# Kernel optimization log

Measured on AMD Instinct MI355X. Metric: run time of the kernel, lower is better.

Reference implementation:

```python
import jax, jax.numpy as jnp
import numpy as np

CR = 0.8
THRESH_FACTOR = 0.05
BN_EPS = 1e-5
NEG_SLOPE = 0.2

@jax.custom_vjp
def ternary(weight, pos, neg):
    # TWN-style ternarization: thresh = f * max|W|
    t = THRESH_FACTOR * jnp.max(jnp.abs(weight))
    pos_i = (weight > t).astype(weight.dtype)
    neg_i = (weight < -t).astype(weight.dtype)
    return pos * pos_i + neg * neg_i

def _tern_fwd(weight, pos, neg):
    t = THRESH_FACTOR * jnp.max(jnp.abs(weight))
    pos_i = (weight > t).astype(weight.dtype)
    neg_i = (weight < -t).astype(weight.dtype)
    return pos * pos_i + neg * neg_i, (pos_i, neg_i, pos, neg)

def _tern_bwd(res, g):
    # matches torch Function_ternary.backward (STE-style)
    pos_i, neg_i, pos, neg = res
    pruned = 1.0 - pos_i - neg_i
    grad_w = pos * g * pos_i + g * pruned + neg * g * neg_i
    return grad_w, jnp.mean(g * pos_i), jnp.mean(g * neg_i)

ternary.defvjp(_tern_fwd, _tern_bwd)

def setup_inputs() -> dict:
    key = jax.random.key(0)
    ks = jax.random.split(key, 6)
    B, Cin, H, W = 32, 256, 64, 64
    Cout, K = 512, 4
    return {
        "x": jax.random.normal(ks[0], (B, Cin, H, W), jnp.float32),
        "weight": jax.random.normal(ks[1], (Cout, Cin, K, K), jnp.float32) * 0.05,
        "pos": jax.random.uniform(ks[2], (), jnp.float32),
        "neg": -jax.random.uniform(ks[3], (), jnp.float32),
        "sal_w": jax.random.normal(ks[4], (Cout, Cin), jnp.float32) * 0.05,
        "sal_b": jax.random.normal(ks[5], (Cout,), jnp.float32) * 0.01,
        "gamma": jnp.ones((Cout,), jnp.float32),
        "beta": jnp.zeros((Cout,), jnp.float32),
    }

def reference(x, weight, pos, neg, sal_w, sal_b, gamma, beta):
    Cout = weight.shape[0]
    # FBS: per-sample channel saliency from spatially pooled |x|
    sub = jnp.mean(jnp.abs(x), axis=(2, 3))                 # [B, Cin]
    sal = jnp.abs(sub @ sal_w.T + sal_b)                    # [B, Cout]
    k = int(np.round(Cout * CR))
    thr = jax.lax.top_k(sal, k)[0][:, -1]                   # k-th largest per sample
    mask = sal * (sal > thr[:, None]).astype(x.dtype)       # [B, Cout]
    # ternary-quantized conv, stride 2, pad 1 (hardcoded in source)
    tw = ternary(weight, pos, neg)
    y = jax.lax.conv_general_dilated(
        x, tw, window_strides=(2, 2), padding=[(1, 1), (1, 1)],
        dimension_numbers=("NCHW", "OIHW", "NCHW"))          # [B, Cout, 32, 32]
    y = mask[:, :, None, None] * y
    # BatchNorm2d (training-mode batch statistics, eps=1e-5)
    mu = jnp.mean(y, axis=(0, 2, 3), keepdims=True)
    var = jnp.var(y, axis=(0, 2, 3), keepdims=True)
    y = (y - mu) * jax.lax.rsqrt(var + BN_EPS)
    y = y * gamma[None, :, None, None] + beta[None, :, None, None]
    # LeakyReLU(0.2)
    return jnp.where(y > 0, y, NEG_SLOPE * y)
```

## Files before the change

### kernel.cpp

```cpp
#include <hip/hip_runtime.h>
#include <stdint.h>

typedef __attribute__((ext_vector_type(8))) short short8;
typedef __attribute__((ext_vector_type(4))) float f32x4;
typedef __attribute__((ext_vector_type(4))) uint32_t u32x4;
typedef __attribute__((ext_vector_type(4))) unsigned short u16x4;

#define K_TOP 410

#define WS_ABSMAX 0
#define WS_GSUM   1024
#define WS_GSQ    3072
#define WS_SCALE  5120
#define WS_SHIFT  7168
#define WS_SUB    16384
#define WS_MASK   65536
#define WS_BMAT   131072

__device__ __forceinline__ unsigned short f2bf(float f) {
  uint32_t u = __float_as_uint(f);
  u += 0x7fffu + ((u >> 16) & 1u);
  return (unsigned short)(u >> 16);
}

__device__ __forceinline__ uint32_t pkbf(float a, float b) {
  uint32_t r;
  asm("v_cvt_pk_bf16_f32 %0, %1, %2" : "=v"(r) : "v"(a), "v"(b));
  return r;
}

__global__ void k_sub(const float* __restrict__ x, float* __restrict__ sub) {
  int bid = blockIdx.x;
  const f32x4* xp = (const f32x4*)(x + (size_t)bid * 4096);
  int t = threadIdx.x;
  float s = 0.f;
#pragma unroll
  for (int i = 0; i < 4; ++i) {
    f32x4 v = xp[t + i * 256];
    s += fabsf(v.x) + fabsf(v.y) + fabsf(v.z) + fabsf(v.w);
  }
#pragma unroll
  for (int off = 32; off > 0; off >>= 1) s += __shfl_xor(s, off);
  __shared__ float red[4];
  if ((t & 63) == 0) red[t >> 6] = s;
  __syncthreads();
  if (t == 0) sub[bid] = (red[0] + red[1] + red[2] + red[3]) * (1.f / 4096.f);
}

__global__ void k_wmax(const float* __restrict__ w, unsigned int* __restrict__ wsmax) {
  int t = blockIdx.x * 256 + threadIdx.x;
  const f32x4* wp = (const f32x4*)w;
  float m = 0.f;
#pragma unroll
  for (int i = 0; i < 8; ++i) {
    f32x4 v = wp[t + i * 65536];
    m = fmaxf(m, fmaxf(fmaxf(fabsf(v.x), fabsf(v.y)), fmaxf(fabsf(v.z), fabsf(v.w))));
  }
#pragma unroll
  for (int off = 32; off > 0; off >>= 1) m = fmaxf(m, __shfl_xor(m, off));
  __shared__ float red[4];
  if ((threadIdx.x & 63) == 0) red[threadIdx.x >> 6] = m;
  __syncthreads();
  if (threadIdx.x == 0) {
    m = fmaxf(fmaxf(red[0], red[1]), fmaxf(red[2], red[3]));
    atomicMax(wsmax, __float_as_uint(m));
  }
}

__global__ void k_mask(const float* __restrict__ sub, const float* __restrict__ salw,
                       const float* __restrict__ salb, float* __restrict__ mask) {
  int b = blockIdx.x, n = threadIdx.x;
  __shared__ float subs[256];
  __shared__ float sals[512];
  __shared__ float thr_s;
  if (n < 256) subs[n] = sub[b * 256 + n];
  __syncthreads();
  float acc = salb[n];
#pragma unroll 4
  for (int c = 0; c < 256; ++c) acc += subs[c] * salw[n * 256 + c];
  float sal = fabsf(acc);
  sals[n] = sal;
  __syncthreads();
  int gt = 0, eq = 0;
  for (int j = 0; j < 512; ++j) {
    float v = sals[j];
    gt += (v > sal);
    eq += (v == sal);
  }
  if (gt < K_TOP && gt + eq >= K_TOP) thr_s = sal;
  __syncthreads();
  mask[b * 512 + n] = (sal > thr_s) ? sal : 0.f;
}

__global__ void k_quant(const float* __restrict__ w, const unsigned int* __restrict__ wsmax,
                        const float* __restrict__ posp, const float* __restrict__ negp,
                        unsigned short* __restrict__ bmat2) {
  int id = blockIdx.x * 256 + threadIdx.x;
  int c = id & 2047;
  int ktq = (id >> 11) & 63;
  int ntq = id >> 17;
  int n = c >> 3, sp = c & 7;
  int s = sp ^ (n & 7);
  int cout = ntq * 256 + n;
  const float* src = w + (size_t)cout * 4096 + ktq * 64 + s * 8;
  float thr = 0.05f * __uint_as_float(*wsmax);
  unsigned short bp = f2bf(*posp), bn = f2bf(*negp);
  f32x4 a = *(const f32x4*)src;
  f32x4 bq = *(const f32x4*)(src + 4);
  u16x4 q0, q1;
  q0.x = a.x > thr ? bp : (a.x < -thr ? bn : (unsigned short)0);
  q0.y = a.y > thr ? bp : (a.y < -thr ? bn : (unsigned short)0);
  q0.z = a.z > thr ? bp : (a.z < -thr ? bn : (unsigned short)0);
  q0.w = a.w > thr ? bp : (a.w < -thr ? bn : (unsigned short)0);
  q1.x = bq.x > thr ? bp : (bq.x < -thr ? bn : (unsigned short)0);
  q1.y = bq.y > thr ? bp : (bq.y < -thr ? bn : (unsigned short)0);
  q1.z = bq.z > thr ? bp : (bq.z < -thr ? bn : (unsigned short)0);
  q1.w = bq.w > thr ? bp : (bq.w < -thr ? bn : (unsigned short)0);
  ((u16x4*)bmat2)[id * 2]     = q0;
  ((u16x4*)bmat2)[id * 2 + 1] = q1;
}

__launch_bounds__(512, 2)
__global__ void k_gemm(const float* __restrict__ x, const unsigned short* __restrict__ bmat2,
                       const float* __restrict__ mask, float* __restrict__ out,
                       float* __restrict__ gsum, float* __restrict__ gsq) {
  __shared__ __align__(16) unsigned short xsL[2][36 * 32 * 8];
  __shared__ __align__(16) unsigned short bsL[2][2048 * 8];

  int tid = threadIdx.x;
  int lane = tid & 63, wid = tid >> 6;
  int wm = wid >> 2, wn = wid & 3;
  int g = lane >> 4, lr = lane & 15;

  int wg = blockIdx.x;
  int nt = wg & 1, mt = wg >> 1;
  int b = mt >> 2, OH0 = (mt & 3) * 8;
  const size_t xb = (size_t)b * 256 * 4096;

  int jA = tid & 15, riA = tid >> 4;
  int c2A = riA / 9, rpA = riA - c2A * 9;
  int ihA = 2 * (OH0 + rpA) - 1;
  bool vA0 = (unsigned)ihA < 64u, vA1 = (unsigned)(ihA + 1) < 64u;
  const float* pA = x + xb + (size_t)c2A * 4096 + (long)ihA * 64 + 4 * jA;
  bool hasB = (wid < 4) && (lane < 16);
  int riB = 32 + wid, jB = lane;
  int rpB = riB - 27;
  int ihB = 2 * (OH0 + rpB) - 1;
  bool vB0 = (unsigned)ihB < 64u, vB1 = (unsigned)(ihB + 1) < 64u;
  const float* pB = x + xb + (size_t)3 * 4096 + (long)ihB * 64 + 4 * jB;

  f32x4 acc[8][4];
#pragma unroll
  for (int i = 0; i < 8; ++i)
#pragma unroll
    for (int j = 0; j < 4; ++j) acc[i][j] = (f32x4){0.f, 0.f, 0.f, 0.f};

  auto ldrow = [&](const float* p, bool v, int j, f32x4& vv, float& pw, float& nx) {
    vv = (f32x4){0.f, 0.f, 0.f, 0.f}; pw = 0.f; nx = 0.f;
    if (v) {
      vv = *(const f32x4*)p;
      if (j != 0)  pw = p[-1];
      if (j != 15) nx = p[4];
    }
  };
  auto wtask = [&](int buf, int rowidx, int j, const f32x4& v0, const f32x4& v1,
                   float pw0, float nx0, float pw1, float nx1) {
    uint32_t a0 = pkbf(pw0, v0.x), b0 = pkbf(v0.y, v0.z), c0 = pkbf(v0.w, nx0);
    uint32_t a1 = pkbf(pw1, v1.x), b1 = pkbf(v1.y, v1.z), c1 = pkbf(v1.w, nx1);
    u32x4* dst = (u32x4*)&xsL[buf][0];
    dst[rowidx * 32 + j]      = (u32x4){a0, b0, a1, b1};
    dst[rowidx * 32 + 16 + j] = (u32x4){b0, c0, b1, c1};
  };
  auto stageB = [&](int buf, int kt) {
    size_t gbase = (size_t)(nt * 64 + kt) * 2048 * 8;
    int wbase = tid & ~63;
#pragma unroll
    for (int q = 0; q < 4; ++q) {
      __builtin_amdgcn_global_load_lds(
          (const uint32_t*)(bmat2 + gbase + (size_t)(q * 512 + tid) * 8),
          (uint32_t*)&bsL[buf][(size_t)(q * 512 + wbase) * 8], 16, 0, 0);
    }
  };

  {
    f32x4 t0v0, t0v1, t1v0, t1v1;
    float t0pw0, t0nx0, t0pw1, t0nx1, t1pw0, t1nx0, t1pw1, t1nx1;
    ldrow(pA, vA0, jA, t0v0, t0pw0, t0nx0);
    ldrow(pA + 64, vA1, jA, t0v1, t0pw1, t0nx1);
    if (hasB) {
      ldrow(pB, vB0, jB, t1v0, t1pw0, t1nx0);
      ldrow(pB + 64, vB1, jB, t1v1, t1pw1, t1nx1);
    }
    stageB(0, 0);
    wtask(0, riA, jA, t0v0, t0v1, t0pw0, t0nx0, t0pw1, t0nx1);
    if (hasB) wtask(0, riB, jB, t1v0, t1v1, t1pw0, t1nx0, t1pw1, t1nx1);
  }
  __syncthreads();

  union UF { u32x4 u; short8 s; };

  for (int kt = 0; kt < 64; ++kt) {
    int cur = kt & 1, nxt = cur ^ 1;

    f32x4 t0v0, t0v1, t1v0, t1v1;
    float t0pw0, t0nx0, t0pw1, t0nx1, t1pw0, t1nx0, t1pw1, t1nx1;
    if (kt < 63) {
      const float* p0 = pA + (size_t)(kt + 1) * 16384;
      ldrow(p0, vA0, jA, t0v0, t0pw0, t0nx0);
      ldrow(p0 + 64, vA1, jA, t0v1, t0pw1, t0nx1);
      if (hasB) {
        const float* p1 = pB + (size_t)(kt + 1) * 16384;
        ldrow(p1, vB0, jB, t1v0, t1pw0, t1nx0);
        ldrow(p1 + 64, vB1, jB, t1v1, t1pw1, t1nx1);
      }
      stageB(nxt, kt + 1);
    }

    const u32x4* xp4 = (const u32x4*)&xsL[cur][0];
    const u32x4* bp4 = (const u32x4*)&bsL[cur][0];
#pragma unroll
    for (int kk = 0; kk < 2; ++kk) {
      UF bf[4];
#pragma unroll
      for (int ni = 0; ni < 4; ++ni) {
        int nloc = wn * 64 + ni * 16 + lr;
        bf[ni].u = bp4[nloc * 8 + ((4 * kk + g) ^ (nloc & 7))];
      }
      __builtin_amdgcn_s_setprio(1);
#pragma unroll
      for (int mi = 0; mi < 8; ++mi) {
        int rowidx = (2 * kk + (g >> 1)) * 9 + wm * 4 + (mi >> 1) + (g & 1);
        int ow = ((mi & 1) << 4) + lr;
        UF af; af.u = xp4[rowidx * 32 + (ow >> 1) + ((ow & 1) << 4)];
#pragma unroll
        for (int ni = 0; ni < 4; ++ni)
          acc[mi][ni] = __builtin_amdgcn_mfma_f32_16x16x32_bf16(af.s, bf[ni].s, acc[mi][ni], 0, 0, 0);
      }
      __builtin_amdgcn_s_setprio(0);
    }

    if (kt < 63) {
      wtask(nxt, riA, jA, t0v0, t0v1, t0pw0, t0nx0, t0pw1, t0nx1);
      if (hasB) wtask(nxt, riB, jB, t1v0, t1v1, t1pw0, t1nx0, t1pw1, t1nx1);
    }
    __syncthreads();
  }

  float msk[4];
#pragma unroll
  for (int ni = 0; ni < 4; ++ni)
    msk[ni] = mask[b * 512 + nt * 256 + wn * 64 + ni * 16 + lr];

  float psum[4] = {0.f, 0.f, 0.f, 0.f}, psq[4] = {0.f, 0.f, 0.f, 0.f};
#pragma unroll
  for (int ni = 0; ni < 4; ++ni) {
    int n = nt * 256 + wn * 64 + ni * 16 + lr;
    float* op = out + (size_t)b * 524288 + (size_t)n * 1024 + OH0 * 32 + wm * 128 + g * 4;
#pragma unroll
    for (int mi = 0; mi < 8; ++mi) {
      f32x4 a = acc[mi][ni] * msk[ni];
      psum[ni] += a.x + a.y + a.z + a.w;
      psq[ni] += a.x * a.x + a.y * a.y + a.z * a.z + a.w * a.w;
      *(f32x4*)(op + mi * 16) = a;
    }
  }
#pragma unroll
  for (int ni = 0; ni < 4; ++ni) {
    float s = psum[ni], q = psq[ni];
    s += __shfl_xor(s, 16); s += __shfl_xor(s, 32);
    q += __shfl_xor(q, 16); q += __shfl_xor(q, 32);
    if (g == 0) {
      int n = nt * 256 + wn * 64 + ni * 16 + lr;
      atomicAdd(&gsum[n], s);
      atomicAdd(&gsq[n], q);
    }
  }
}

__global__ void k_bnprep(const float* __restrict__ gsum, const float* __restrict__ gsq,
                         const float* __restrict__ gamma, const float* __restrict__ beta,
                         float* __restrict__ scale, float* __restrict__ shift) {
  int n = threadIdx.x;
  float mu = gsum[n] * (1.f / 32768.f);
  float var = gsq[n] * (1.f / 32768.f) - mu * mu;
  float a = gamma[n] * rsqrtf(var + 1e-5f);
  scale[n] = a;
  shift[n] = beta[n] - mu * a;
}

__global__ void k_bn(float* __restrict__ y, const float* __restrict__ scale,
                     const float* __restrict__ shift) {
  int t = blockIdx.x * 256 + threadIdx.x;
  f32x4* yp = (f32x4*)y;
#pragma unroll
  for (int i = 0; i < 8; ++i) {
    int idx = t + i * 524288;
    int n = (idx >> 8) & 511;
    f32x4 v = yp[idx];
    float a = scale[n], sh = shift[n];
    v = v * a + sh;
    v.x = v.x > 0.f ? v.x : 0.2f * v.x;
    v.y = v.y > 0.f ? v.y : 0.2f * v.y;
    v.z = v.z > 0.f ? v.z : 0.2f * v.z;
    v.w = v.w > 0.f ? v.w : 0.2f * v.w;
    yp[idx] = v;
  }
}

extern "C" void kernel_launch(void* const* d_in, const int* in_sizes, int n_in,
                              void* d_out, int out_size, void* d_ws, size_t ws_size,
                              hipStream_t stream) {
  const float* x     = (const float*)d_in[0];
  const float* w     = (const float*)d_in[1];
  const float* pos   = (const float*)d_in[2];
  const float* neg   = (const float*)d_in[3];
  const float* salw  = (const float*)d_in[4];
  const float* salb  = (const float*)d_in[5];
  const float* gamma = (const float*)d_in[6];
  const float* beta  = (const float*)d_in[7];
  float* out = (float*)d_out;
  char* ws = (char*)d_ws;

  unsigned int* absmax = (unsigned int*)(ws + WS_ABSMAX);
  float* gsum  = (float*)(ws + WS_GSUM);
  float* gsq   = (float*)(ws + WS_GSQ);
  float* scale = (float*)(ws + WS_SCALE);
  float* shift = (float*)(ws + WS_SHIFT);
  float* sub   = (float*)(ws + WS_SUB);
  float* mask  = (float*)(ws + WS_MASK);
  unsigned short* bmat2 = (unsigned short*)(ws + WS_BMAT);

  hipMemsetAsync(ws, 0, 5120, stream);

  k_sub<<<8192, 256, 0, stream>>>(x, sub);
  k_wmax<<<256, 256, 0, stream>>>(w, absmax);
  k_mask<<<32, 512, 0, stream>>>(sub, salw, salb, mask);
  k_quant<<<1024, 256, 0, stream>>>(w, absmax, pos, neg, bmat2);
  k_gemm<<<256, 512, 0, stream>>>(x, bmat2, mask, out, gsum, gsq);
  k_bnprep<<<1, 512, 0, stream>>>(gsum, gsq, gamma, beta, scale, shift);
  k_bn<<<2048, 256, 0, stream>>>(out, scale, shift);
}
```

Measured before the change: 462.6 us.

## Use lane shuffles for halo values, batch LDS reads, and hand-tune barriers

The row loader now fetches only the aligned f32x4 per lane and gets the neighbouring halo elements through __shfl_up/__shfl_down, so the two scalar global loads per row go away. All A-fragments are read from LDS before the MFMA burst. __syncthreads is replaced by an explicit waitcnt, s_barrier and sched_barrier, plus an extra barrier in the middle of the k-steps. The workgroup-to-tile mapping also changes so that consecutive blocks share the same N tile instead of alternating between the two. This adds shuffle work and register pressure from holding eight A-fragments, and the extra mid-loop barrier could add stalls.

After: 419.4 us. 1.1x faster.

```diff
diff --git a/kernel.cpp b/kernel.cpp
--- a/kernel.cpp
+++ b/kernel.cpp
@@ -133,7 +133,7 @@
   int g = lane >> 4, lr = lane & 15;
 
   int wg = blockIdx.x;
-  int nt = wg & 1, mt = wg >> 1;
+  int nt = wg >> 7, mt = wg & 127;
   int b = mt >> 2, OH0 = (mt & 3) * 8;
   const size_t xb = (size_t)b * 256 * 4096;
 
@@ -143,7 +143,7 @@
   bool vA0 = (unsigned)ihA < 64u, vA1 = (unsigned)(ihA + 1) < 64u;
   const float* pA = x + xb + (size_t)c2A * 4096 + (long)ihA * 64 + 4 * jA;
   bool hasB = (wid < 4) && (lane < 16);
-  int riB = 32 + wid, jB = lane;
+  int riB = 32 + wid, jB = lane & 15;
   int rpB = riB - 27;
   int ihB = 2 * (OH0 + rpB) - 1;
   bool vB0 = (unsigned)ihB < 64u, vB1 = (unsigned)(ihB + 1) < 64u;
@@ -155,16 +155,13 @@
 #pragma unroll
     for (int j = 0; j < 4; ++j) acc[i][j] = (f32x4){0.f, 0.f, 0.f, 0.f};
 
-  auto ldrow = [&](const float* p, bool v, int j, f32x4& vv, float& pw, float& nx) {
-    vv = (f32x4){0.f, 0.f, 0.f, 0.f}; pw = 0.f; nx = 0.f;
-    if (v) {
-      vv = *(const f32x4*)p;
-      if (j != 0)  pw = p[-1];
-      if (j != 15) nx = p[4];
-    }
-  };
-  auto wtask = [&](int buf, int rowidx, int j, const f32x4& v0, const f32x4& v1,
-                   float pw0, float nx0, float pw1, float nx1) {
+  auto z4 = []() { return (f32x4){0.f, 0.f, 0.f, 0.f}; };
+
+  auto wtask = [&](int buf, int rowidx, int j, f32x4 v0, f32x4 v1) {
+    float pw0 = __shfl_up(v0.w, 1);  if (j == 0)  pw0 = 0.f;
+    float nx0 = __shfl_down(v0.x, 1); if (j == 15) nx0 = 0.f;
+    float pw1 = __shfl_up(v1.w, 1);  if (j == 0)  pw1 = 0.f;
+    float nx1 = __shfl_down(v1.x, 1); if (j == 15) nx1 = 0.f;
     uint32_t a0 = pkbf(pw0, v0.x), b0 = pkbf(v0.y, v0.z), c0 = pkbf(v0.w, nx0);
     uint32_t a1 = pkbf(pw1, v1.x), b1 = pkbf(v1.y, v1.z), c1 = pkbf(v1.w, nx1);
     u32x4* dst = (u32x4*)&xsL[buf][0];
@@ -182,36 +179,37 @@
     }
   };
 
+  union UF { u32x4 u; short8 s; };
+
   {
-    f32x4 t0v0, t0v1, t1v0, t1v1;
-    float t0pw0, t0nx0, t0pw1, t0nx1, t1pw0, t1nx0, t1pw1, t1nx1;
-    ldrow(pA, vA0, jA, t0v0, t0pw0, t0nx0);
-    ldrow(pA + 64, vA1, jA, t0v1, t0pw1, t0nx1);
+    f32x4 a0 = vA0 ? *(const f32x4*)pA : z4();
+    f32x4 a1 = vA1 ? *(const f32x4*)(pA + 64) : z4();
+    f32x4 c0 = z4(), c1 = z4();
     if (hasB) {
-      ldrow(pB, vB0, jB, t1v0, t1pw0, t1nx0);
-      ldrow(pB + 64, vB1, jB, t1v1, t1pw1, t1nx1);
+      c0 = vB0 ? *(const f32x4*)pB : z4();
+      c1 = vB1 ? *(const f32x4*)(pB + 64) : z4();
     }
     stageB(0, 0);
-    wtask(0, riA, jA, t0v0, t0v1, t0pw0, t0nx0, t0pw1, t0nx1);
-    if (hasB) wtask(0, riB, jB, t1v0, t1v1, t1pw0, t1nx0, t1pw1, t1nx1);
-  }
-  __syncthreads();
-
-  union UF { u32x4 u; short8 s; };
+    wtask(0, riA, jA, a0, a1);
+    if (hasB) wtask(0, riB, jB, c0, c1);
+    asm volatile("s_waitcnt vmcnt(0) lgkmcnt(0)" ::: "memory");
+    __builtin_amdgcn_s_barrier();
+    __builtin_amdgcn_sched_barrier(0);
+  }
 
   for (int kt = 0; kt < 64; ++kt) {
     int cur = kt & 1, nxt = cur ^ 1;
-
-    f32x4 t0v0, t0v1, t1v0, t1v1;
-    float t0pw0, t0nx0, t0pw1, t0nx1, t1pw0, t1nx0, t1pw1, t1nx1;
-    if (kt < 63) {
+    bool pre = (kt < 63);
+
+    f32x4 a0, a1, c0, c1;
+    if (pre) {
       const float* p0 = pA + (size_t)(kt + 1) * 16384;
-      ldrow(p0, vA0, jA, t0v0, t0pw0, t0nx0);
-      ldrow(p0 + 64, vA1, jA, t0v1, t0pw1, t0nx1);
+      a0 = vA0 ? *(const f32x4*)p0 : z4();
+      a1 = vA1 ? *(const f32x4*)(p0 + 64) : z4();
       if (hasB) {
         const float* p1 = pB + (size_t)(kt + 1) * 16384;
-        ldrow(p1, vB0, jB, t1v0, t1pw0, t1nx0);
-        ldrow(p1 + 64, vB1, jB, t1v1, t1pw1, t1nx1);
+        c0 = vB0 ? *(const f32x4*)p1 : z4();
+        c1 = vB1 ? *(const f32x4*)(p1 + 64) : z4();
       }
       stageB(nxt, kt + 1);
     }
@@ -226,24 +224,30 @@
         int nloc = wn * 64 + ni * 16 + lr;
         bf[ni].u = bp4[nloc * 8 + ((4 * kk + g) ^ (nloc & 7))];
       }
-      __builtin_amdgcn_s_setprio(1);
+      UF af[8];
 #pragma unroll
       for (int mi = 0; mi < 8; ++mi) {
         int rowidx = (2 * kk + (g >> 1)) * 9 + wm * 4 + (mi >> 1) + (g & 1);
         int ow = ((mi & 1) << 4) + lr;
-        UF af; af.u = xp4[rowidx * 32 + (ow >> 1) + ((ow & 1) << 4)];
+        af[mi].u = xp4[rowidx * 32 + (ow >> 1) + ((ow & 1) << 4)];
+      }
+      __builtin_amdgcn_s_setprio(1);
+#pragma unroll
+      for (int mi = 0; mi < 8; ++mi)
 #pragma unroll
         for (int ni = 0; ni < 4; ++ni)
-          acc[mi][ni] = __builtin_amdgcn_mfma_f32_16x16x32_bf16(af.s, bf[ni].s, acc[mi][ni], 0, 0, 0);
-      }
+          acc[mi][ni] = __builtin_amdgcn_mfma_f32_16x16x32_bf16(af[mi].s, bf[ni].s, acc[mi][ni], 0, 0, 0);
       __builtin_amdgcn_s_setprio(0);
-    }
-
-    if (kt < 63) {
-      wtask(nxt, riA, jA, t0v0, t0v1, t0pw0, t0nx0, t0pw1, t0nx1);
-      if (hasB) wtask(nxt, riB, jB, t1v0, t1v1, t1pw0, t1nx0, t1pw1, t1nx1);
-    }
-    __syncthreads();
+      if (kk == 0) __builtin_amdgcn_s_barrier();
+    }
+
+    if (pre) {
+      wtask(nxt, riA, jA, a0, a1);
+      if (hasB) wtask(nxt, riB, jB, c0, c1);
+    }
+    asm volatile("s_waitcnt vmcnt(0) lgkmcnt(0)" ::: "memory");
+    __builtin_amdgcn_s_barrier();
+    __builtin_amdgcn_sched_barrier(0);
   }
 
   float msk[4];
```
